# Performance work log

Hardware: AMD Instinct MI355X
Metric: run time of the kernel (lower is better)

## Reference

```python
import jax, jax.numpy as jnp
import numpy as np

EMBED_DIM = 768
NUM_HEADS = 12
HEAD_DIM = EMBED_DIM // NUM_HEADS
B, S = 2, 2048


def setup_inputs() -> dict:
    key = jax.random.key(0)
    k1, k2, k3, k4, k5 = jax.random.split(key, 5)
    scale = 1.0 / np.sqrt(EMBED_DIM)
    return {
        "x": jax.random.normal(k1, (B, S, EMBED_DIM), dtype=jnp.float32),
        "w_qkv": jax.random.normal(k2, (EMBED_DIM, 3 * EMBED_DIM), dtype=jnp.float32) * scale,
        "b_qkv": jax.random.normal(k3, (3 * EMBED_DIM,), dtype=jnp.float32) * 0.01,
        "w_proj": jax.random.normal(k4, (EMBED_DIM, EMBED_DIM), dtype=jnp.float32) * scale,
        "b_proj": jax.random.normal(k5, (EMBED_DIM,), dtype=jnp.float32) * 0.01,
    }


def reference(x, w_qkv, b_qkv, w_proj, b_proj):
    b, s, e = x.shape
    h, d = NUM_HEADS, HEAD_DIM
    # fused QKV projection: [b, s, 3, h, d]
    qkv = (x @ w_qkv + b_qkv).reshape(b, s, 3, h, d)
    q = qkv[:, :, 0].transpose(0, 2, 1, 3)  # [b, h, s, d]
    k = qkv[:, :, 1].transpose(0, 2, 1, 3)
    v = qkv[:, :, 2].transpose(0, 2, 1, 3)
    scores = jnp.einsum("bhqd,bhkd->bhqk", q, k) * (d ** -0.5)
    attn = jax.nn.softmax(scores, axis=-1)  # dropout is identity in eval mode
    out = jnp.einsum("bhqk,bhkd->bhqd", attn, v)
    out = out.transpose(0, 2, 1, 3).reshape(b, s, e)
    return out @ w_proj + b_proj
```

## Files before the change

### kernel.cpp

```cpp
#include <hip/hip_runtime.h>
#include <hip/hip_bf16.h>


typedef __bf16 bf16x8 __attribute__((ext_vector_type(8)));
typedef float f32x4 __attribute__((ext_vector_type(4)));
typedef unsigned short ushortx8 __attribute__((ext_vector_type(8)));
typedef unsigned short ushortx4 __attribute__((ext_vector_type(4)));

#define EMB 768
#define SEQ 2048
#define NHEAD 12
#define HDIM 64
#define MROWS 4096
#define NQKV 2304
#define QSCALE 0.18033688011112042f

static __device__ __forceinline__ unsigned short b16(float f) {
  __hip_bfloat16 h = __float2bfloat16(f);
  return __builtin_bit_cast(unsigned short, h);
}

static __device__ __forceinline__ void gld16(const void* g, void* l) {
  __builtin_amdgcn_global_load_lds((const __attribute__((address_space(1))) void*)g,
                                   (__attribute__((address_space(3))) void*)l, 16, 0, 0);
}

__global__ __launch_bounds__(256) void k_prep(
    const float* __restrict__ x, const float* __restrict__ wqkv, const float* __restrict__ wproj,
    unsigned short* __restrict__ xb, unsigned short* __restrict__ wqkvT,
    unsigned short* __restrict__ wprojT) {
  __shared__ float t[64][65];
  const int bid = blockIdx.x;
  if (bid < 3072) {
    int i = (bid * 256 + threadIdx.x) * 4;
    f32x4 v = *(const f32x4*)(x + i);
    ushortx4 o;
    o[0] = b16(v[0]); o[1] = b16(v[1]); o[2] = b16(v[2]); o[3] = b16(v[3]);
    *(ushortx4*)(xb + i) = o;
    return;
  }
  const float* in; unsigned short* out; int N, bx, by;
  if (bid < 3072 + 432) { in = wqkv;  out = wqkvT;  N = NQKV; int r = bid - 3072; bx = r % 36; by = r / 36; }
  else                  { in = wproj; out = wprojT; N = EMB;  int r = bid - 3504; bx = r % 12; by = r / 12; }
  const int n0 = bx * 64, k0 = by * 64;
  const int xx = threadIdx.x & 63, y0 = threadIdx.x >> 6;
  #pragma unroll
  for (int i = 0; i < 16; ++i) { int r = y0 * 16 + i; t[r][xx] = in[(size_t)(k0 + r) * N + n0 + xx]; }
  __syncthreads();
  #pragma unroll
  for (int i = 0; i < 16; ++i) { int r = y0 * 16 + i; out[(size_t)(n0 + r) * EMB + k0 + xx] = b16(t[xx][r]); }
}

static __device__ __forceinline__ void gemm_tile_128(
    const unsigned short* __restrict__ A, const unsigned short* __restrict__ B,
    int K, int bm, int bn, char* lA, char* lB, f32x4 acc[4][4]) {
  const int tid = threadIdx.x, lane = tid & 63, w = tid >> 6;
  const int l15 = lane & 15, lg = lane >> 4;
  const int wm = w >> 1, wn = w & 1;
  #pragma unroll
  for (int m = 0; m < 4; ++m)
    #pragma unroll
    for (int n = 0; n < 4; ++n)
      acc[m][n] = (f32x4){0.f, 0.f, 0.f, 0.f};

  const int srow = w * 32 + (lane >> 3);
  const int glog = (lane & 7) ^ (lane >> 3);
  const size_t abase = (size_t)(bm * 128 + srow) * K + glog * 8;
  const size_t bbase = (size_t)(bn * 128 + srow) * K + glog * 8;
  const char* aB = lA + (wm * 64 + l15) * 128;
  const char* bB = lB + (wn * 64 + l15) * 128;
  const int rsw = (l15 & 7) << 4;

  const int T = K >> 6;
  {
    char* ad = lA + w * 4096; char* bd = lB + w * 4096;
    #pragma unroll
    for (int j = 0; j < 4; ++j) {
      gld16(A + abase + (size_t)j * 8 * K, ad + j * 1024);
      gld16(B + bbase + (size_t)j * 8 * K, bd + j * 1024);
    }
  }
  for (int t = 0; t < T; ++t) {
    const int cur = t & 1;
    if (t + 1 < T) {
      const int k1 = (t + 1) << 6;
      char* ad = lA + (cur ^ 1) * 16384 + w * 4096;
      char* bd = lB + (cur ^ 1) * 16384 + w * 4096;
      #pragma unroll
      for (int j = 0; j < 4; ++j) {
        gld16(A + abase + (size_t)j * 8 * K + k1, ad + j * 1024);
        gld16(B + bbase + (size_t)j * 8 * K + k1, bd + j * 1024);
      }
      asm volatile("s_waitcnt vmcnt(8)" ::: "memory");
    } else {
      asm volatile("s_waitcnt vmcnt(0)" ::: "memory");
    }
    __builtin_amdgcn_s_barrier();
    const char* ab = aB + cur * 16384;
    const char* bb = bB + cur * 16384;
    bf16x8 af[2][4], bfr[2][4];
    #pragma unroll
    for (int kk = 0; kk < 2; ++kk) {
      #pragma unroll
      for (int m = 0; m < 4; ++m)
        af[kk][m] = *(const bf16x8*)(ab + m * 2048 + (((kk * 4 + lg) * 16) ^ rsw));
      #pragma unroll
      for (int n = 0; n < 4; ++n)
        bfr[kk][n] = *(const bf16x8*)(bb + n * 2048 + (((kk * 4 + lg) * 16) ^ rsw));
    }
    #pragma unroll
    for (int kk = 0; kk < 2; ++kk)
      #pragma unroll
      for (int m = 0; m < 4; ++m)
        #pragma unroll
        for (int n = 0; n < 4; ++n)
          acc[m][n] = __builtin_amdgcn_mfma_f32_16x16x32_bf16(af[kk][m], bfr[kk][n], acc[m][n], 0, 0, 0);
    if (t + 1 < T) __builtin_amdgcn_s_barrier();
  }
}

static __device__ __forceinline__ int kvperm(int s) {
  return (s & ~0x1C) | ((s & 0x0C) << 1) | ((s & 0x10) >> 2);
}

__global__ __launch_bounds__(256) void k_gemm_qkv(
    const unsigned short* __restrict__ Xb, const unsigned short* __restrict__ Wt,
    const float* __restrict__ bias,
    unsigned short* __restrict__ Qb, unsigned short* __restrict__ Kb,
    unsigned short* __restrict__ VTb) {
  __shared__ __align__(16) char Alds[2 * 16384];
  __shared__ __align__(16) char Blds[2 * 16384];
  f32x4 acc[4][4];
  const int bm = blockIdx.x, bn = blockIdx.y;
  gemm_tile_128(Xb, Wt, EMB, bm, bn, Alds, Blds, acc);
  const int tid = threadIdx.x, lane = tid & 63, w = tid >> 6;
  const int l15 = lane & 15, lg = lane >> 4, wm = w >> 1, wn = w & 1;
  const int treg = bn / 6;
  if (treg < 2) {
    #pragma unroll
    for (int m = 0; m < 4; ++m)
      #pragma unroll
      for (int n = 0; n < 4; ++n)
        #pragma unroll
        for (int r = 0; r < 4; ++r) {
          int gr = bm * 128 + wm * 64 + m * 16 + lg * 4 + r;
          int gc = bn * 128 + wn * 64 + n * 16 + l15;
          float v = acc[m][n][r] + bias[gc];
          int rem = gc - treg * 768;
          int h = rem >> 6, d = rem & 63;
          int b = gr >> 11, s = gr & 2047;
          size_t off = ((size_t)(b * 12 + h) * 2048 + s) * 64 + d;
          if (treg == 0) Qb[off] = b16(v * QSCALE);
          else           Kb[off] = b16(v);
        }
  } else {
    #pragma unroll
    for (int m = 0; m < 4; ++m)
      #pragma unroll
      for (int n = 0; n < 4; ++n) {
        int gr0 = bm * 128 + wm * 64 + m * 16 + lg * 4;
        int gc = bn * 128 + wn * 64 + n * 16 + l15;
        int rem = gc - 1536;
        int h = rem >> 6, d = rem & 63;
        int b = gr0 >> 11, s0 = gr0 & 2047;
        int sp0 = kvperm(s0);
        ushortx4 o;
        #pragma unroll
        for (int r = 0; r < 4; ++r) o[r] = b16(acc[m][n][r] + bias[gc]);
        *(ushortx4*)(VTb + ((size_t)(b * 12 + h) * 64 + d) * 2048 + sp0) = o;
      }
  }
}

__global__ __launch_bounds__(256) void k_gemm_proj(
    const unsigned short* __restrict__ Ab, const unsigned short* __restrict__ Wt,
    const float* __restrict__ bias, float* __restrict__ out) {
  __shared__ __align__(16) char Alds[2 * 16384];
  __shared__ __align__(16) char Blds[2 * 16384];
  f32x4 acc[4][4];
  const int bm = blockIdx.x, bn = blockIdx.y;
  gemm_tile_128(Ab, Wt, EMB, bm, bn, Alds, Blds, acc);
  const int tid = threadIdx.x, lane = tid & 63, w = tid >> 6;
  const int l15 = lane & 15, lg = lane >> 4, wm = w >> 1, wn = w & 1;
  #pragma unroll
  for (int m = 0; m < 4; ++m)
    #pragma unroll
    for (int n = 0; n < 4; ++n)
      #pragma unroll
      for (int r = 0; r < 4; ++r) {
        int gr = bm * 128 + wm * 64 + m * 16 + lg * 4 + r;
        int gc = bn * 128 + wn * 64 + n * 16 + l15;
        out[(size_t)gr * EMB + gc] = acc[m][n][r] + bias[gc];
      }
}

__global__ __launch_bounds__(256) void k_attn(
    const unsigned short* __restrict__ Qg, const unsigned short* __restrict__ Kg,
    const unsigned short* __restrict__ VTg, unsigned short* __restrict__ AO) {
  __shared__ __align__(16) char KL[3 * 8192];
  __shared__ __align__(16) char VTL[3 * 8192];
  const int bid = blockIdx.x;
  const int slot = bid >> 3;
  const int bh = (bid & 7) * 3 + slot / 32;
  const int qt = slot & 31;
  const int b = bh / 12, h = bh % 12;
  const size_t base = (size_t)bh * (SEQ * HDIM);
  const int tid = threadIdx.x, lane = tid & 63, w = tid >> 6;
  const int l15 = lane & 15, lg = lane >> 4;
  const int swz = (l15 & 7) << 4;

  bf16x8 qf[2];
  {
    const size_t qoff = base + (size_t)(qt * 64 + w * 16 + l15) * 64 + lg * 8;
    qf[0] = *(const bf16x8*)(Qg + qoff);
    qf[1] = *(const bf16x8*)(Qg + qoff + 32);
  }

  const int srow0 = tid >> 3;
  const int scg0 = (tid & 7) ^ (srow0 & 7);
  const int scg1 = (tid & 7) ^ ((srow0 + 32) & 7);

  #define ASTAGE(tt, buf) do {                                                         \
    const int kv_ = (tt) * 64;                                                         \
    char* kd_ = KL + (buf) * 8192 + w * 1024;                                          \
    char* vd_ = VTL + (buf) * 8192 + w * 1024;                                         \
    gld16(Kg + base + (size_t)(kv_ + srow0) * 64 + scg0 * 8,           kd_);           \
    gld16(Kg + base + (size_t)(kv_ + srow0 + 32) * 64 + scg1 * 8,      kd_ + 4096);    \
    gld16(VTg + base + (size_t)srow0 * 2048 + kv_ + scg0 * 8,          vd_);           \
    gld16(VTg + base + (size_t)(srow0 + 32) * 2048 + kv_ + scg1 * 8,   vd_ + 4096);    \
  } while (0)

  f32x4 Oacc[4];
  #pragma unroll
  for (int nd = 0; nd < 4; ++nd) Oacc[nd] = (f32x4){0.f, 0.f, 0.f, 0.f};
  float l_ = 0.f;

  ASTAGE(0, 0);
  ASTAGE(1, 1);
  asm volatile("s_waitcnt vmcnt(4)" ::: "memory");
  __builtin_amdgcn_s_barrier();

  int cur = 0, pre = 2;
  for (int t = 0; t < 32; ++t) {
    if (t + 2 < 32) ASTAGE(t + 2, pre);
    const char* kb = KL + cur * 8192;
    const char* vb = VTL + cur * 8192;

    f32x4 sv[4];
    __builtin_amdgcn_s_setprio(1);
    #pragma unroll
    for (int n = 0; n < 4; ++n) {
      const char* rb = kb + (n * 16 + l15) * 128;
      bf16x8 kf0 = *(const bf16x8*)(rb + ((lg * 16) ^ swz));
      bf16x8 kf1 = *(const bf16x8*)(rb + ((64 + lg * 16) ^ swz));
      f32x4 z = (f32x4){0.f, 0.f, 0.f, 0.f};
      z = __builtin_amdgcn_mfma_f32_16x16x32_bf16(kf0, qf[0], z, 0, 0, 0);
      sv[n] = __builtin_amdgcn_mfma_f32_16x16x32_bf16(kf1, qf[1], z, 0, 0, 0);
    }

    #pragma unroll
    for (int c = 0; c < 2; ++c) {
      ushortx8 up;
      #pragma unroll
      for (int j = 0; j < 4; ++j) {
        float pa = __builtin_amdgcn_exp2f(sv[2 * c][j]);
        float pb = __builtin_amdgcn_exp2f(sv[2 * c + 1][j]);
        l_ += pa + pb;
        up[j] = b16(pa);
        up[4 + j] = b16(pb);
      }
      bf16x8 pfB = __builtin_bit_cast(bf16x8, up);
      #pragma unroll
      for (int nd = 0; nd < 4; ++nd) {
        const char* vr = vb + (nd * 16 + l15) * 128;
        bf16x8 vf = *(const bf16x8*)(vr + ((c * 64 + lg * 16) ^ swz));
        Oacc[nd] = __builtin_amdgcn_mfma_f32_16x16x32_bf16(vf, pfB, Oacc[nd], 0, 0, 0);
      }
    }
    __builtin_amdgcn_s_setprio(0);

    if (t < 31) {
      if (t < 30) asm volatile("s_waitcnt vmcnt(4)" ::: "memory");
      else        asm volatile("s_waitcnt vmcnt(0)" ::: "memory");
      __builtin_amdgcn_s_barrier();
    }
    cur = (cur == 2) ? 0 : cur + 1;
    pre = (pre == 2) ? 0 : pre + 1;
  }
  #undef ASTAGE

  l_ += __shfl_xor(l_, 16);
  l_ += __shfl_xor(l_, 32);
  const float rl = 1.0f / l_;
  const int q = qt * 64 + w * 16 + l15;
  #pragma unroll
  for (int nd = 0; nd < 4; ++nd) {
    ushortx4 o;
    #pragma unroll
    for (int r = 0; r < 4; ++r) o[r] = b16(Oacc[nd][r] * rl);
    *(ushortx4*)(AO + ((size_t)(b * 2048 + q)) * EMB + h * 64 + nd * 16 + lg * 4) = o;
  }
}

extern "C" void kernel_launch(void* const* d_in, const int* in_sizes, int n_in,
                              void* d_out, int out_size, void* d_ws, size_t ws_size,
                              hipStream_t stream) {
  const float* x     = (const float*)d_in[0];
  const float* wqkv  = (const float*)d_in[1];
  const float* bqkv  = (const float*)d_in[2];
  const float* wproj = (const float*)d_in[3];
  const float* bproj = (const float*)d_in[4];
  float* out = (float*)d_out;
  char* ws = (char*)d_ws;

  unsigned short* xb     = (unsigned short*)(ws + 0);
  unsigned short* wqkvT  = (unsigned short*)(ws + 6291456);
  unsigned short* wprojT = (unsigned short*)(ws + 9830400);
  unsigned short* Qb     = (unsigned short*)(ws + 11010048);
  unsigned short* Kb     = (unsigned short*)(ws + 17301504);
  unsigned short* VTb    = (unsigned short*)(ws + 23592960);
  unsigned short* AOb    = (unsigned short*)(ws + 29884416);

  k_prep<<<3648, 256, 0, stream>>>(x, wqkv, wproj, xb, wqkvT, wprojT);
  k_gemm_qkv<<<dim3(MROWS / 128, NQKV / 128), 256, 0, stream>>>(xb, wqkvT, bqkv, Qb, Kb, VTb);
  k_attn<<<24 * (SEQ / 64), 256, 0, stream>>>(Qb, Kb, VTb, AOb);
  k_gemm_proj<<<dim3(MROWS / 128, EMB / 128), 256, 0, stream>>>(AOb, wprojT, bproj, out);
}
```

Before: 89.23 us.

## Use 32x32 MFMA in attention with split-KV across waves and MFMA row sums

Result: slower. 92.85 us (+4.1%).

```diff
diff --git a/kernel.cpp b/kernel.cpp
--- a/kernel.cpp
+++ b/kernel.cpp
@@ -4,6 +4,7 @@
 
 typedef __bf16 bf16x8 __attribute__((ext_vector_type(8)));
 typedef float f32x4 __attribute__((ext_vector_type(4)));
+typedef float f32x16 __attribute__((ext_vector_type(16)));
 typedef unsigned short ushortx8 __attribute__((ext_vector_type(8)));
 typedef unsigned short ushortx4 __attribute__((ext_vector_type(4)));
 
@@ -120,7 +121,7 @@
 }
 
 static __device__ __forceinline__ int kvperm(int s) {
-  return (s & ~0x1C) | ((s & 0x0C) << 1) | ((s & 0x10) >> 2);
+  return (s & ~12) | ((s & 4) << 1) | ((s & 8) >> 1);
 }
 
 __global__ __launch_bounds__(256) void k_gemm_qkv(
@@ -206,14 +207,15 @@
   const int b = bh / 12, h = bh % 12;
   const size_t base = (size_t)bh * (SEQ * HDIM);
   const int tid = threadIdx.x, lane = tid & 63, w = tid >> 6;
-  const int l15 = lane & 15, lg = lane >> 4;
-  const int swz = (l15 & 7) << 4;
-
-  bf16x8 qf[2];
+  const int l31 = lane & 31, g = lane >> 5;
+  const int qh = w >> 1, kh = w & 1;
+  const int swz = (lane & 7) << 4;
+
+  bf16x8 qf[4];
   {
-    const size_t qoff = base + (size_t)(qt * 64 + w * 16 + l15) * 64 + lg * 8;
-    qf[0] = *(const bf16x8*)(Qg + qoff);
-    qf[1] = *(const bf16x8*)(Qg + qoff + 32);
+    const size_t qoff = base + (size_t)(qt * 64 + qh * 32 + l31) * 64 + g * 8;
+    #pragma unroll
+    for (int dc = 0; dc < 4; ++dc) qf[dc] = *(const bf16x8*)(Qg + qoff + dc * 16);
   }
 
   const int srow0 = tid >> 3;
@@ -230,10 +232,19 @@
     gld16(VTg + base + (size_t)(srow0 + 32) * 2048 + kv_ + scg1 * 8,   vd_ + 4096);    \
   } while (0)
 
-  f32x4 Oacc[4];
-  #pragma unroll
-  for (int nd = 0; nd < 4; ++nd) Oacc[nd] = (f32x4){0.f, 0.f, 0.f, 0.f};
-  float l_ = 0.f;
+  ushortx8 os;
+  #pragma unroll
+  for (int j = 0; j < 8; ++j) os[j] = 0x3F80;
+  const bf16x8 onesf = __builtin_bit_cast(bf16x8, os);
+
+  f32x16 Oacc[2];
+  #pragma unroll
+  for (int dh = 0; dh < 2; ++dh)
+    #pragma unroll
+    for (int j = 0; j < 16; ++j) Oacc[dh][j] = 0.f;
+  f32x16 Lacc;
+  #pragma unroll
+  for (int j = 0; j < 16; ++j) Lacc[j] = 0.f;
 
   ASTAGE(0, 0);
   ASTAGE(1, 1);
@@ -246,40 +257,42 @@
     const char* kb = KL + cur * 8192;
     const char* vb = VTL + cur * 8192;
 
-    f32x4 sv[4];
     __builtin_amdgcn_s_setprio(1);
-    #pragma unroll
-    for (int n = 0; n < 4; ++n) {
-      const char* rb = kb + (n * 16 + l15) * 128;
-      bf16x8 kf0 = *(const bf16x8*)(rb + ((lg * 16) ^ swz));
-      bf16x8 kf1 = *(const bf16x8*)(rb + ((64 + lg * 16) ^ swz));
-      f32x4 z = (f32x4){0.f, 0.f, 0.f, 0.f};
-      z = __builtin_amdgcn_mfma_f32_16x16x32_bf16(kf0, qf[0], z, 0, 0, 0);
-      sv[n] = __builtin_amdgcn_mfma_f32_16x16x32_bf16(kf1, qf[1], z, 0, 0, 0);
-    }
-
-    #pragma unroll
-    for (int c = 0; c < 2; ++c) {
-      ushortx8 up;
-      #pragma unroll
-      for (int j = 0; j < 4; ++j) {
-        float pa = __builtin_amdgcn_exp2f(sv[2 * c][j]);
-        float pb = __builtin_amdgcn_exp2f(sv[2 * c + 1][j]);
-        l_ += pa + pb;
-        up[j] = b16(pa);
-        up[4 + j] = b16(pb);
-      }
-      bf16x8 pfB = __builtin_bit_cast(bf16x8, up);
-      #pragma unroll
-      for (int nd = 0; nd < 4; ++nd) {
-        const char* vr = vb + (nd * 16 + l15) * 128;
-        bf16x8 vf = *(const bf16x8*)(vr + ((c * 64 + lg * 16) ^ swz));
-        Oacc[nd] = __builtin_amdgcn_mfma_f32_16x16x32_bf16(vf, pfB, Oacc[nd], 0, 0, 0);
-      }
+    f32x16 sv;
+    #pragma unroll
+    for (int j = 0; j < 16; ++j) sv[j] = 0.f;
+    {
+      const char* krow = kb + (kh * 32 + l31) * 128;
+      #pragma unroll
+      for (int dc = 0; dc < 4; ++dc) {
+        bf16x8 kf = *(const bf16x8*)(krow + ((dc * 32 + g * 16) ^ swz));
+        sv = __builtin_amdgcn_mfma_f32_32x32x16_bf16(kf, qf[dc], sv, 0, 0, 0);
+      }
+    }
+
+    ushortx8 u0, u1;
+    #pragma unroll
+    for (int j = 0; j < 8; ++j) {
+      u0[j] = b16(__builtin_amdgcn_exp2f(sv[j]));
+      u1[j] = b16(__builtin_amdgcn_exp2f(sv[8 + j]));
+    }
+    const bf16x8 pf0 = __builtin_bit_cast(bf16x8, u0);
+    const bf16x8 pf1 = __builtin_bit_cast(bf16x8, u1);
+    Lacc = __builtin_amdgcn_mfma_f32_32x32x16_bf16(onesf, pf0, Lacc, 0, 0, 0);
+    Lacc = __builtin_amdgcn_mfma_f32_32x32x16_bf16(onesf, pf1, Lacc, 0, 0, 0);
+
+    #pragma unroll
+    for (int dh = 0; dh < 2; ++dh) {
+      const char* vrow = vb + (dh * 32 + l31) * 128;
+      bf16x8 vf0 = *(const bf16x8*)(vrow + ((kh * 64 + g * 16) ^ swz));
+      bf16x8 vf1 = *(const bf16x8*)(vrow + ((kh * 64 + 32 + g * 16) ^ swz));
+      Oacc[dh] = __builtin_amdgcn_mfma_f32_32x32x16_bf16(vf0, pf0, Oacc[dh], 0, 0, 0);
+      Oacc[dh] = __builtin_amdgcn_mfma_f32_32x32x16_bf16(vf1, pf1, Oacc[dh], 0, 0, 0);
     }
     __builtin_amdgcn_s_setprio(0);
 
     if (t < 31) {
+      asm volatile("s_waitcnt lgkmcnt(0)" ::: "memory");
       if (t < 30) asm volatile("s_waitcnt vmcnt(4)" ::: "memory");
       else        asm volatile("s_waitcnt vmcnt(0)" ::: "memory");
       __builtin_amdgcn_s_barrier();
@@ -289,16 +302,34 @@
   }
   #undef ASTAGE
 
-  l_ += __shfl_xor(l_, 16);
-  l_ += __shfl_xor(l_, 32);
-  const float rl = 1.0f / l_;
-  const int q = qt * 64 + w * 16 + l15;
-  #pragma unroll
-  for (int nd = 0; nd < 4; ++nd) {
-    ushortx4 o;
-    #pragma unroll
-    for (int r = 0; r < 4; ++r) o[r] = b16(Oacc[nd][r] * rl);
-    *(ushortx4*)(AO + ((size_t)(b * 2048 + q)) * EMB + h * 64 + nd * 16 + lg * 4) = o;
+  asm volatile("s_waitcnt lgkmcnt(0) vmcnt(0)" ::: "memory");
+  __builtin_amdgcn_s_barrier();
+  float* xch = (float*)KL;
+  const int li = qh * 64 + lane;
+  if (kh == 1) {
+    float* dst = xch + li * 33;
+    #pragma unroll
+    for (int dh = 0; dh < 2; ++dh)
+      #pragma unroll
+      for (int j = 0; j < 16; ++j) dst[dh * 16 + j] = Oacc[dh][j];
+    dst[32] = Lacc[0];
+  }
+  __syncthreads();
+  if (kh == 0) {
+    const float* src = xch + li * 33;
+    const float rl = 1.0f / (Lacc[0] + src[32]);
+    const int q = qt * 64 + qh * 32 + l31;
+    unsigned short* aor = AO + ((size_t)(b * 2048 + q)) * EMB + h * 64;
+    #pragma unroll
+    for (int dh = 0; dh < 2; ++dh)
+      #pragma unroll
+      for (int rg = 0; rg < 4; ++rg) {
+        ushortx4 o;
+        #pragma unroll
+        for (int rr = 0; rr < 4; ++rr)
+          o[rr] = b16((Oacc[dh][rg * 4 + rr] + src[dh * 16 + rg * 4 + rr]) * rl);
+        *(ushortx4*)(aor + dh * 32 + rg * 8 + g * 4) = o;
+      }
   }
 }
 
```
